# Kernel tuning notes

Hardware: AMD Instinct MI355X
Metric: run time of the kernel (lower is better)

Reference implementation:

```python
import jax, jax.numpy as jnp
import numpy as np

N_NODES = 100000
N_EDGES = 1600000
DIM_IN = 128
DIM_OUT = 64


def _spmm(edge_row, edge_col, edge_vals, X):
    # DAD.mm(X): sparse COO [N,N] times dense [N,d]
    # gather source features, scale by edge value, scatter-add to rows
    msgs = edge_vals[:, None] * X[edge_col]          # [E, d]
    return jax.ops.segment_sum(msgs, edge_row, num_segments=N_NODES)


def setup_inputs() -> dict:
    key = jax.random.key(0)
    k1, k2, k3, k4, k5, k6 = jax.random.split(key, 6)
    X = jax.random.normal(k1, (N_NODES, DIM_IN), dtype=jnp.float32)
    W1 = jax.random.normal(k2, (DIM_IN, DIM_IN), dtype=jnp.float32) * (1.0 / np.sqrt(DIM_IN))
    W2 = jax.random.normal(k3, (DIM_OUT, DIM_IN), dtype=jnp.float32) * (1.0 / np.sqrt(DIM_IN))
    edge_vals = jax.random.uniform(k4, (N_EDGES,), dtype=jnp.float32)
    edge_row = jax.random.randint(k5, (N_EDGES,), 0, N_NODES, dtype=jnp.int32)
    edge_col = jax.random.randint(k6, (N_EDGES,), 0, N_NODES, dtype=jnp.int32)
    return {"X": X, "W1": W1, "W2": W2, "edge_vals": edge_vals,
            "edge_row": edge_row, "edge_col": edge_col}


def reference(X, W1, W2, edge_vals, edge_row, edge_col):
    # layer 1: tanh(fc1(DAD @ X)); nn.Linear(bias=False) is x @ W.T
    h = jnp.tanh(_spmm(edge_row, edge_col, edge_vals, X) @ W1.T)
    # layer 2: tanh(fc2(DAD @ h))
    out = jnp.tanh(_spmm(edge_row, edge_col, edge_vals, h) @ W2.T)
    return out
```

## Files before the change

### kernel.cpp

```cpp
#include <hip/hip_runtime.h>
#include <hip/hip_bf16.h>
#include <hip/hip_fp16.h>

#define N_NODES 100000
#define N_EDGES 1600000
#define DIM_IN 128
#define DIM_OUT 64

#define NB 391
#define NCHUNK 391
#define CHUNK 4096
#define BCAP 5120

typedef unsigned int uint;
typedef unsigned short ushort;
typedef _Float16 half8 __attribute__((ext_vector_type(8)));
typedef float f32x4 __attribute__((ext_vector_type(4)));

__device__ inline ushort f2h(float f) {
    __half h = __float2half(f);
    return *reinterpret_cast<ushort*>(&h);
}


__global__ __launch_bounds__(256) void chunk_hist_kernel(const int* __restrict__ erow,
                                                         int* __restrict__ counts, int E) {
    __shared__ int hist[NB];
    const int t = threadIdx.x, c = blockIdx.x;
    for (int b = t; b < NB; b += 256) hist[b] = 0;
    __syncthreads();
    const int eb = c * CHUNK;
#pragma unroll
    for (int i = 0; i < CHUNK / 256; ++i) {
        int e = eb + i * 256 + t;
        if (e < E) atomicAdd(&hist[erow[e] >> 8], 1);
    }
    __syncthreads();
    for (int b = t; b < NB; b += 256) counts[b * NCHUNK + c] = hist[b];
}

__global__ __launch_bounds__(512) void bucket_scan_kernel(const int* __restrict__ counts,
                                                          int* __restrict__ offnb,
                                                          int* __restrict__ tot) {
    __shared__ int s[512];
    const int b = blockIdx.x, t = threadIdx.x;
    int v = (t < NCHUNK) ? counts[b * NCHUNK + t] : 0;
    s[t] = v;
    __syncthreads();
#pragma unroll
    for (int o = 1; o < 512; o <<= 1) {
        int x = s[t];
        int y = (t >= o) ? s[t - o] : 0;
        __syncthreads();
        s[t] = x + y;
        __syncthreads();
    }
    if (t < NCHUNK) offnb[b * NCHUNK + t] = s[t] - v;
    if (t == 511) tot[b] = s[511];
}

__global__ __launch_bounds__(512) void base_scan_kernel(const int* __restrict__ tot,
                                                        int* __restrict__ bbase) {
    __shared__ int s[512];
    const int t = threadIdx.x;
    int v = (t < NB) ? tot[t] : 0;
    s[t] = v;
    __syncthreads();
#pragma unroll
    for (int o = 1; o < 512; o <<= 1) {
        int x = s[t];
        int y = (t >= o) ? s[t - o] : 0;
        __syncthreads();
        s[t] = x + y;
        __syncthreads();
    }
    if (t < NB) bbase[t] = s[t] - v;
    if (t == 511) bbase[NB] = s[511];
}

__global__ __launch_bounds__(512) void coarse_scatter_kernel(const int* __restrict__ erow,
                                                             const int* __restrict__ ecol,
                                                             const float* __restrict__ eval,
                                                             const int* __restrict__ offnb,
                                                             const int* __restrict__ bbase,
                                                             uint* __restrict__ keyOut,
                                                             float* __restrict__ valOut, int E) {
    __shared__ int hist[NB];
    __shared__ int segOff[NB];
    __shared__ int localOff[NB];
    __shared__ int sc[512];
    __shared__ int idxL[CHUNK];
    __shared__ int gaddrL[CHUNK];

    const int t = threadIdx.x, c = blockIdx.x;
    for (int b = t; b < NB; b += 512) {
        hist[b] = 0;
        segOff[b] = bbase[b] + offnb[b * NCHUNK + c];
    }
    __syncthreads();
    const int eb = c * CHUNK;
    uint bq[CHUNK / 512];
#pragma unroll
    for (int i = 0; i < CHUNK / 512; ++i) {
        int e = eb + i * 512 + t;
        if (e < E) {
            int b = erow[e] >> 8;
            int q = atomicAdd(&hist[b], 1);
            bq[i] = ((uint)b << 16) | (uint)q;
        } else {
            bq[i] = 0xFFFFFFFFu;
        }
    }
    __syncthreads();
    int v = (t < NB) ? hist[t] : 0;
    sc[t] = v;
    __syncthreads();
#pragma unroll
    for (int o = 1; o < 512; o <<= 1) {
        int x = sc[t];
        int y = (t >= o) ? sc[t - o] : 0;
        __syncthreads();
        sc[t] = x + y;
        __syncthreads();
    }
    if (t < NB) localOff[t] = sc[t] - v;
    __syncthreads();
#pragma unroll
    for (int i = 0; i < CHUNK / 512; ++i) {
        if (bq[i] != 0xFFFFFFFFu) {
            int b = bq[i] >> 16;
            int q = bq[i] & 0xFFFF;
            int s = localOff[b] + q;
            idxL[s] = eb + i * 512 + t;
            gaddrL[s] = segOff[b] + q;
        }
    }
    __syncthreads();
    const int m = min(CHUNK, E - eb);
    for (int s = t; s < m; s += 512) {
        int e = idxL[s];
        int g = gaddrL[s];
        keyOut[g] = ((uint)(erow[e] & 255) << 17) | (uint)ecol[e];
        valOut[g] = eval[e];
    }
}

__global__ __launch_bounds__(256) void fine_sort_kernel(const uint* __restrict__ keyOut,
                                                        const float* __restrict__ valOut,
                                                        const int* __restrict__ bbase,
                                                        int* __restrict__ row_ptr,
                                                        int2* __restrict__ ep) {
    __shared__ uint keyL[BCAP];
    __shared__ int hist[256];
    __shared__ int offs[256];
    const int b = blockIdx.x, t = threadIdx.x;
    const int s0 = bbase[b], s1 = bbase[b + 1];
    const int m = min(s1 - s0, BCAP);
    hist[t] = 0;
    __syncthreads();
    for (int j = t; j < m; j += 256) {
        uint k = keyOut[s0 + j];
        keyL[j] = k;
        atomicAdd(&hist[k >> 17], 1);
    }
    __syncthreads();
    int v = hist[t];
    offs[t] = v;
    __syncthreads();
#pragma unroll
    for (int o = 1; o < 256; o <<= 1) {
        int x = offs[t];
        int y = (t >= o) ? offs[t - o] : 0;
        __syncthreads();
        offs[t] = x + y;
        __syncthreads();
    }
    int excl = offs[t] - v;
    int row = b * 256 + t;
    if (row < N_NODES) row_ptr[row] = s0 + excl;
    if (b == NB - 1 && t == 0) row_ptr[N_NODES] = s1;
    hist[t] = excl;
    __syncthreads();
    for (int j = t; j < m; j += 256) {
        uint k = keyL[j];
        int pos = atomicAdd(&hist[k >> 17], 1);
        float vv = valOut[s0 + j];
        ep[s0 + pos] = make_int2((int)(k & 0x1FFFFu), __float_as_int(vv));
    }
}


__global__ __launch_bounds__(256) void cvt_f16_kernel(const float* __restrict__ in,
                                                      uint* __restrict__ outp, int n8) {
    int i = blockIdx.x * 256 + threadIdx.x;
    if (i >= n8) return;
    const float4* in4 = reinterpret_cast<const float4*>(in) + (size_t)i * 2;
    float4 a = in4[0];
    float4 b = in4[1];
    uint4 o;
    o.x = (uint)f2h(a.x) | ((uint)f2h(a.y) << 16);
    o.y = (uint)f2h(a.z) | ((uint)f2h(a.w) << 16);
    o.z = (uint)f2h(b.x) | ((uint)f2h(b.y) << 16);
    o.w = (uint)f2h(b.z) | ((uint)f2h(b.w) << 16);
    reinterpret_cast<uint4*>(outp)[i] = o;
}


template <int NOUT, bool TANH, bool AF32>
__global__ __launch_bounds__(256) void mfma_gemm_kernel(const void* __restrict__ Ain,
                                                        const uint* __restrict__ Wh,
                                                        uint* __restrict__ Out, int M) {
    constexpr int CF = NOUT / 16;
    __shared__ __align__(16) ushort sA[128 * 128];
    __shared__ __align__(16) ushort sB[NOUT * 128];

    const int t = threadIdx.x;
    const int l = t & 63;
    const int w = t >> 6;
    const int row0 = blockIdx.x * 128;
    const int lr = l & 15;
    const int lk = l >> 4;

    if (AF32) {
        const float* Af = (const float*)Ain;
#pragma unroll
        for (int i = 0; i < 16; ++i) {
            int fid = i * 256 + t;
            int row = fid >> 5, q4 = fid & 31;
            int gr = row0 + row;
            float4 v = make_float4(0.f, 0.f, 0.f, 0.f);
            if (gr < M) v = *reinterpret_cast<const float4*>(Af + (size_t)gr * 128 + q4 * 4);
            uint2 p;
            p.x = (uint)f2h(v.x) | ((uint)f2h(v.y) << 16);
            p.y = (uint)f2h(v.z) | ((uint)f2h(v.w) << 16);
            int slot = q4 >> 1;
            *reinterpret_cast<uint2*>(&sA[row * 128 + ((slot ^ (row & 7)) << 3) + (q4 & 1) * 4]) = p;
        }
    } else {
        const uint4* A4 = (const uint4*)Ain;
#pragma unroll
        for (int i = 0; i < 8; ++i) {
            int fid = i * 256 + t;
            int row = fid >> 4, slot = fid & 15;
            int gr = row0 + row;
            uint4 v = make_uint4(0, 0, 0, 0);
            if (gr < M) v = A4[(size_t)gr * 16 + slot];
            *reinterpret_cast<uint4*>(&sA[row * 128 + ((slot ^ (row & 7)) << 3)]) = v;
        }
    }
#pragma unroll
    for (int i = 0; i < NOUT / 16; ++i) {
        int fid = i * 256 + t;
        int row = fid >> 4, slot = fid & 15;
        uint4 v = reinterpret_cast<const uint4*>(Wh)[row * 16 + slot];
        *reinterpret_cast<uint4*>(&sB[row * 128 + ((slot ^ (row & 7)) << 3)]) = v;
    }
    __syncthreads();

    f32x4 acc[2][CF];
#pragma unroll
    for (int rf = 0; rf < 2; ++rf)
#pragma unroll
        for (int cf = 0; cf < CF; ++cf) acc[rf][cf] = (f32x4){0.f, 0.f, 0.f, 0.f};

    half8 aF[2][4];
#pragma unroll
    for (int rf = 0; rf < 2; ++rf) {
        int row = w * 32 + rf * 16 + lr;
#pragma unroll
        for (int kc = 0; kc < 4; ++kc) {
            int slot = kc * 4 + lk;
            aF[rf][kc] = *reinterpret_cast<const half8*>(&sA[row * 128 + ((slot ^ (row & 7)) << 3)]);
        }
    }
#pragma unroll
    for (int cf = 0; cf < CF; ++cf) {
        int col = cf * 16 + lr;
#pragma unroll
        for (int kc = 0; kc < 4; ++kc) {
            int slot = kc * 4 + lk;
            half8 bF = *reinterpret_cast<const half8*>(&sB[col * 128 + ((slot ^ (col & 7)) << 3)]);
            acc[0][cf] = __builtin_amdgcn_mfma_f32_16x16x32_f16(aF[0][kc], bF, acc[0][cf], 0, 0, 0);
            acc[1][cf] = __builtin_amdgcn_mfma_f32_16x16x32_f16(aF[1][kc], bF, acc[1][cf], 0, 0, 0);
        }
    }
    __syncthreads();

    ushort* sOut = sA;
#pragma unroll
    for (int rf = 0; rf < 2; ++rf)
#pragma unroll
        for (int cf = 0; cf < CF; ++cf)
#pragma unroll
            for (int reg = 0; reg < 4; ++reg) {
                int row = w * 32 + rf * 16 + lk * 4 + reg;
                int col = cf * 16 + lr;
                float x = acc[rf][cf][reg];
                sOut[row * NOUT + col] = f2h(TANH ? tanhf(x) : x);
            }
    __syncthreads();
    constexpr int QPR = NOUT / 8;
#pragma unroll
    for (int i = 0; i < 128 * QPR / 256; ++i) {
        int fid = i * 256 + t;
        int row = fid / QPR, q = fid % QPR;
        int gr = row0 + row;
        if (gr < M)
            reinterpret_cast<uint4*>(Out)[(size_t)gr * QPR + q] =
                *reinterpret_cast<const uint4*>(&sOut[row * NOUT + q * 8]);
    }
}


__global__ __launch_bounds__(256) void spmm1_kernel(const int2* __restrict__ ep,
                                                    const int* __restrict__ row_ptr,
                                                    const uint* __restrict__ T,
                                                    uint* __restrict__ Hh) {
    int wave = threadIdx.x >> 6;
    int lane = threadIdx.x & 63;
    int r = blockIdx.x * 4 + wave;
    if (r >= N_NODES) return;
    int beg = row_ptr[r];
    int end = row_ptr[r + 1];
    if (beg >= end) {
        Hh[(size_t)r * 64 + lane] = 0u;
        return;
    }
    float a0x = 0.f, a0y = 0.f, a1x = 0.f, a1y = 0.f;
    for (int e = beg; e < end; e += 8) {
        int2 cv[8];
        uint xu[8];
#pragma unroll
        for (int i = 0; i < 8; ++i) {
            int idx = (e + i < end) ? e + i : end - 1;
            cv[i] = ep[idx];
        }
#pragma unroll
        for (int i = 0; i < 8; ++i) xu[i] = T[(size_t)cv[i].x * 64 + lane];
#pragma unroll
        for (int i = 0; i < 8; ++i) {
            float v = (e + i < end) ? __int_as_float(cv[i].y) : 0.f;
            __half2 h2 = *reinterpret_cast<__half2*>(&xu[i]);
            float2 f = __half22float2(h2);
            if (i & 1) { a1x += v * f.x; a1y += v * f.y; }
            else       { a0x += v * f.x; a0y += v * f.y; }
        }
    }
    Hh[(size_t)r * 64 + lane] =
        (uint)f2h(tanhf(a0x + a1x)) | ((uint)f2h(tanhf(a0y + a1y)) << 16);
}


__global__ __launch_bounds__(256) void spmm2_kernel(const int2* __restrict__ ep,
                                                    const int* __restrict__ row_ptr,
                                                    const ushort* __restrict__ Ph,
                                                    float* __restrict__ out) {
    int wave = threadIdx.x >> 6;
    int lane = threadIdx.x & 63;
    int r = blockIdx.x * 4 + wave;
    if (r >= N_NODES) return;
    int beg = row_ptr[r];
    int end = row_ptr[r + 1];
    if (beg >= end) {
        out[(size_t)r * DIM_OUT + lane] = 0.f;
        return;
    }
    float acc0 = 0.f, acc1 = 0.f;
    for (int e = beg; e < end; e += 8) {
        int2 cv[8];
        ushort xu[8];
#pragma unroll
        for (int i = 0; i < 8; ++i) {
            int idx = (e + i < end) ? e + i : end - 1;
            cv[i] = ep[idx];
        }
#pragma unroll
        for (int i = 0; i < 8; ++i) xu[i] = Ph[(size_t)cv[i].x * 64 + lane];
#pragma unroll
        for (int i = 0; i < 8; ++i) {
            float v = (e + i < end) ? __int_as_float(cv[i].y) : 0.f;
            __half h = *reinterpret_cast<__half*>(&xu[i]);
            float x = __half2float(h);
            if (i & 1) acc1 += v * x;
            else       acc0 += v * x;
        }
    }
    out[(size_t)r * DIM_OUT + lane] = tanhf(acc0 + acc1);
}


extern "C" void kernel_launch(void* const* d_in, const int* in_sizes, int n_in,
                              void* d_out, int out_size, void* d_ws, size_t ws_size,
                              hipStream_t stream) {
    const float* X = (const float*)d_in[0];
    const float* W1 = (const float*)d_in[1];
    const float* W2 = (const float*)d_in[2];
    const float* evals = (const float*)d_in[3];
    const int* erow = (const int*)d_in[4];
    const int* ecol = (const int*)d_in[5];
    float* out = (float*)d_out;

    const int N = N_NODES;
    const int E = N_EDGES;

    char* ws = (char*)d_ws;
    size_t off = 0;
    auto alloc = [&](size_t bytes) {
        size_t o = off;
        off = (off + bytes + 255) & ~(size_t)255;
        return o;
    };
    size_t o_counts = alloc((size_t)NB * NCHUNK * 4);
    size_t o_offnb = alloc((size_t)NB * NCHUNK * 4);
    size_t o_tot = alloc((size_t)NB * 4);
    size_t o_bbase = alloc((size_t)(NB + 1) * 4);
    size_t o_rowptr = alloc((size_t)(N + 1) * 4);
    size_t o_ep = alloc((size_t)E * 8);
    size_t o_key = alloc((size_t)E * 4);
    size_t o_val = alloc((size_t)E * 4);
    size_t o_xw1 = alloc((size_t)N * 64 * 4);
    size_t o_hh = alloc((size_t)N * 64 * 4);
    size_t o_ph = alloc((size_t)N * 32 * 4);
    size_t o_w1h = alloc((size_t)128 * 64 * 4);
    size_t o_w2h = alloc((size_t)64 * 64 * 4);
    (void)ws_size;

    int* counts = (int*)(ws + o_counts);
    int* offnb = (int*)(ws + o_offnb);
    int* tot = (int*)(ws + o_tot);
    int* bbase = (int*)(ws + o_bbase);
    int* row_ptr = (int*)(ws + o_rowptr);
    int2* ep = (int2*)(ws + o_ep);
    uint* keyOut = (uint*)(ws + o_key);
    float* valOut = (float*)(ws + o_val);
    uint* XW1h = (uint*)(ws + o_xw1);
    uint* Hh = (uint*)(ws + o_hh);
    uint* Ph = (uint*)(ws + o_ph);
    uint* W1h = (uint*)(ws + o_w1h);
    uint* W2h = (uint*)(ws + o_w2h);

    const int gemm_grid = (N + 127) / 128;
    const int spmm_grid = (N + 3) / 4;

    cvt_f16_kernel<<<8, 256, 0, stream>>>(W1, W1h, 128 * 128 / 8);
    cvt_f16_kernel<<<4, 256, 0, stream>>>(W2, W2h, 64 * 128 / 8);
    mfma_gemm_kernel<128, false, true><<<gemm_grid, 256, 0, stream>>>(X, W1h, XW1h, N);

    chunk_hist_kernel<<<NCHUNK, 256, 0, stream>>>(erow, counts, E);
    bucket_scan_kernel<<<NB, 512, 0, stream>>>(counts, offnb, tot);
    base_scan_kernel<<<1, 512, 0, stream>>>(tot, bbase);
    coarse_scatter_kernel<<<NCHUNK, 512, 0, stream>>>(erow, ecol, evals, offnb, bbase,
                                                      keyOut, valOut, E);
    fine_sort_kernel<<<NB, 256, 0, stream>>>(keyOut, valOut, bbase, row_ptr, ep);

    spmm1_kernel<<<spmm_grid, 256, 0, stream>>>(ep, row_ptr, XW1h, Hh);
    mfma_gemm_kernel<64, false, false><<<gemm_grid, 256, 0, stream>>>(Hh, W2h, Ph, N);
    spmm2_kernel<<<spmm_grid, 256, 0, stream>>>(ep, row_ptr, (const ushort*)Ph, out);
}
```

Baseline: 244.6 us.

## Sort edges within each row by column group and drop padded gathers in SpMM

The fine sort now bins each row's edges by column group (upper bits of the column index), so the edges of a row are ordered roughly by source node. The goal is better locality in the feature gathers of both SpMM passes. The SpMM kernels also stop rounding each row up to a multiple of 8 with redundant clamped loads, and instead use an exact-count tail loop. The cost is a much larger shared histogram (6400 bins) and a 25-element per-thread scan in the sort kernel, which may lower occupancy there.

Result: faster. 236.1 us (-3.5%).

```diff
diff --git a/kernel.cpp b/kernel.cpp
--- a/kernel.cpp
+++ b/kernel.cpp
@@ -11,6 +11,9 @@
 #define NCHUNK 391
 #define CHUNK 4096
 #define BCAP 5120
+#define CGBITS 12
+#define NCG 25
+#define FBINS (256 * NCG)
 
 typedef unsigned int uint;
 typedef unsigned short ushort;
@@ -151,41 +154,49 @@
                                                         int* __restrict__ row_ptr,
                                                         int2* __restrict__ ep) {
     __shared__ uint keyL[BCAP];
-    __shared__ int hist[256];
-    __shared__ int offs[256];
+    __shared__ int hist[FBINS];
+    __shared__ int tsum[256];
     const int b = blockIdx.x, t = threadIdx.x;
     const int s0 = bbase[b], s1 = bbase[b + 1];
     const int m = min(s1 - s0, BCAP);
-    hist[t] = 0;
+    for (int i = t; i < FBINS; i += 256) hist[i] = 0;
     __syncthreads();
     for (int j = t; j < m; j += 256) {
         uint k = keyOut[s0 + j];
         keyL[j] = k;
-        atomicAdd(&hist[k >> 17], 1);
-    }
-    __syncthreads();
-    int v = hist[t];
-    offs[t] = v;
+        int bin = (int)(k >> 17) * NCG + (int)((k & 0x1FFFFu) >> CGBITS);
+        atomicAdd(&hist[bin], 1);
+    }
+    __syncthreads();
+    int loc[NCG];
+    int run = 0;
+#pragma unroll
+    for (int i = 0; i < NCG; ++i) {
+        loc[i] = run;
+        run += hist[t * NCG + i];
+    }
+    tsum[t] = run;
     __syncthreads();
 #pragma unroll
     for (int o = 1; o < 256; o <<= 1) {
-        int x = offs[t];
-        int y = (t >= o) ? offs[t - o] : 0;
-        __syncthreads();
-        offs[t] = x + y;
-        __syncthreads();
-    }
-    int excl = offs[t] - v;
+        int x = tsum[t];
+        int y = (t >= o) ? tsum[t - o] : 0;
+        __syncthreads();
+        tsum[t] = x + y;
+        __syncthreads();
+    }
+    int excl = tsum[t] - run;
     int row = b * 256 + t;
     if (row < N_NODES) row_ptr[row] = s0 + excl;
     if (b == NB - 1 && t == 0) row_ptr[N_NODES] = s1;
-    hist[t] = excl;
+#pragma unroll
+    for (int i = 0; i < NCG; ++i) hist[t * NCG + i] = excl + loc[i];
     __syncthreads();
     for (int j = t; j < m; j += 256) {
         uint k = keyL[j];
-        int pos = atomicAdd(&hist[k >> 17], 1);
-        float vv = valOut[s0 + j];
-        ep[s0 + pos] = make_int2((int)(k & 0x1FFFFu), __float_as_int(vv));
+        int bin = (int)(k >> 17) * NCG + (int)((k & 0x1FFFFu) >> CGBITS);
+        int pos = atomicAdd(&hist[bin], 1);
+        ep[s0 + pos] = make_int2((int)(k & 0x1FFFFu), __float_as_int(valOut[s0 + j]));
     }
 }
 
@@ -322,29 +333,32 @@
     if (r >= N_NODES) return;
     int beg = row_ptr[r];
     int end = row_ptr[r + 1];
-    if (beg >= end) {
-        Hh[(size_t)r * 64 + lane] = 0u;
-        return;
-    }
     float a0x = 0.f, a0y = 0.f, a1x = 0.f, a1y = 0.f;
-    for (int e = beg; e < end; e += 8) {
+    int e = beg;
+    for (; e + 7 < end; e += 8) {
         int2 cv[8];
         uint xu[8];
 #pragma unroll
+        for (int i = 0; i < 8; ++i) cv[i] = ep[e + i];
+#pragma unroll
+        for (int i = 0; i < 8; ++i) xu[i] = T[(size_t)cv[i].x * 64 + lane];
+#pragma unroll
         for (int i = 0; i < 8; ++i) {
-            int idx = (e + i < end) ? e + i : end - 1;
-            cv[i] = ep[idx];
-        }
-#pragma unroll
-        for (int i = 0; i < 8; ++i) xu[i] = T[(size_t)cv[i].x * 64 + lane];
-#pragma unroll
-        for (int i = 0; i < 8; ++i) {
-            float v = (e + i < end) ? __int_as_float(cv[i].y) : 0.f;
+            float v = __int_as_float(cv[i].y);
             __half2 h2 = *reinterpret_cast<__half2*>(&xu[i]);
             float2 f = __half22float2(h2);
             if (i & 1) { a1x += v * f.x; a1y += v * f.y; }
             else       { a0x += v * f.x; a0y += v * f.y; }
         }
+    }
+    for (; e < end; ++e) {
+        int2 cv = ep[e];
+        float v = __int_as_float(cv.y);
+        uint xu = T[(size_t)cv.x * 64 + lane];
+        __half2 h2 = *reinterpret_cast<__half2*>(&xu);
+        float2 f = __half22float2(h2);
+        a0x += v * f.x;
+        a0y += v * f.y;
     }
     Hh[(size_t)r * 64 + lane] =
         (uint)f2h(tanhf(a0x + a1x)) | ((uint)f2h(tanhf(a0y + a1y)) << 16);
@@ -361,29 +375,29 @@
     if (r >= N_NODES) return;
     int beg = row_ptr[r];
     int end = row_ptr[r + 1];
-    if (beg >= end) {
-        out[(size_t)r * DIM_OUT + lane] = 0.f;
-        return;
-    }
     float acc0 = 0.f, acc1 = 0.f;
-    for (int e = beg; e < end; e += 8) {
+    int e = beg;
+    for (; e + 7 < end; e += 8) {
         int2 cv[8];
         ushort xu[8];
 #pragma unroll
+        for (int i = 0; i < 8; ++i) cv[i] = ep[e + i];
+#pragma unroll
+        for (int i = 0; i < 8; ++i) xu[i] = Ph[(size_t)cv[i].x * 64 + lane];
+#pragma unroll
         for (int i = 0; i < 8; ++i) {
-            int idx = (e + i < end) ? e + i : end - 1;
-            cv[i] = ep[idx];
-        }
-#pragma unroll
-        for (int i = 0; i < 8; ++i) xu[i] = Ph[(size_t)cv[i].x * 64 + lane];
-#pragma unroll
-        for (int i = 0; i < 8; ++i) {
-            float v = (e + i < end) ? __int_as_float(cv[i].y) : 0.f;
+            float v = __int_as_float(cv[i].y);
             __half h = *reinterpret_cast<__half*>(&xu[i]);
             float x = __half2float(h);
             if (i & 1) acc1 += v * x;
             else       acc0 += v * x;
         }
+    }
+    for (; e < end; ++e) {
+        int2 cv = ep[e];
+        ushort u = Ph[(size_t)cv.x * 64 + lane];
+        __half h = *reinterpret_cast<__half*>(&u);
+        acc0 += __int_as_float(cv.y) * __half2float(h);
     }
     out[(size_t)r * DIM_OUT + lane] = tanhf(acc0 + acc1);
 }
```
